# Performance work log

Measured on AMD Instinct MI355X. Metric: run time of the kernel, lower is better.

The kernel has to match this reference:

```python
import jax, jax.numpy as jnp
import numpy as np

PD_THR = 1e-6  # positive-definiteness floor for the diagonal covariance

N_IN, DIM, BATCH = 8192, 128, 4096


def setup_inputs() -> dict:
    key = jax.random.key(0)
    kx, km = jax.random.split(key)
    x = jax.random.normal(kx, (BATCH, DIM), dtype=jnp.float32)
    mean = jax.random.normal(km, (N_IN, DIM), dtype=jnp.float32)
    diag = jnp.ones((N_IN, DIM), dtype=jnp.float32)
    return {"x": x, "mean": mean, "diag": diag}


def reference(x, mean, diag):
    """Energies[b, i] = KL( N(x_b, I) || N(mean_i, diag(diag_i)) ).

    Diagonal-Gaussian KL:
      0.5 * sum_d [ log(diag_id) + (1 + (x_bd - mu_id)^2) / diag_id - 1 ]

    The pairwise quadratic term is expanded into GEMMs to avoid the
    (batch, n_in, dim) broadcast intermediate:
      sum_d (x-mu)^2/diag = x^2 @ inv.T - 2 x @ (mu*inv).T + sum(mu^2*inv)
    Returns (batch, n_in), i.e. the original's energies.T.
    """
    d = jnp.clip(diag, PD_THR, None)              # (n_in, dim)
    inv = 1.0 / d                                 # (n_in, dim)
    # pairwise Mahalanobis quadratic, shape (batch, n_in)
    quad = (
        (x * x) @ inv.T
        - 2.0 * (x @ (mean * inv).T)
        + jnp.sum(mean * mean * inv, axis=-1)     # (n_in,) broadcast
    )
    # per-codebook constants: logdet + trace(inv) - dim
    const = jnp.sum(jnp.log(d), axis=-1) + jnp.sum(inv, axis=-1) - x.shape[-1]
    return 0.5 * (quad + const)                   # (batch, n_in)
```

## Files before the change

kernel.cpp:

```cpp
#include <hip/hip_runtime.h>
#include <hip/hip_bf16.h>


#define BATCH 4096
#define N_IN  8192
#define DIM   128
#define KP    768
#define PD_THR 1e-6f

#define BM 256
#define BN 256
#define BK 64
#define NT (KP / BK)

typedef __attribute__((ext_vector_type(4))) float f32x4;
typedef __attribute__((ext_vector_type(8))) short bf16x8;

static __device__ __forceinline__ unsigned short f2bf(float v) {
    union { __hip_bfloat16 h; unsigned short u; } cv;
    cv.h = __float2bfloat16(v);
    return cv.u;
}
static __device__ __forceinline__ float bf2f(unsigned short u) {
    union { unsigned short u; __hip_bfloat16 h; } cv;
    cv.u = u;
    return __bfloat162float(cv.h);
}

__global__ void prep_a_kernel(const float* __restrict__ x,
                              unsigned short* __restrict__ Ap) {
    int t = blockIdx.x * 256 + threadIdx.x;
    int row = t >> 7;
    int d   = t & 127;
    float v  = x[t];
    float x2 = v * v;
    unsigned short x2h = f2bf(x2);
    unsigned short x2l = f2bf(x2 - bf2f(x2h));
    unsigned short xh  = f2bf(v);
    unsigned short xl  = f2bf(v - bf2f(xh));
    unsigned short* a = Ap + (size_t)row * KP;
    a[d]       = x2h;  a[128 + d] = xh;
    a[256 + d] = x2h;  a[384 + d] = xh;
    a[512 + d] = x2l;  a[640 + d] = xl;
}

__global__ void prep_b_kernel(const float* __restrict__ mean,
                              const float* __restrict__ diag,
                              unsigned short* __restrict__ Bp,
                              float* __restrict__ cvec) {
    int wave = threadIdx.x >> 6, lane = threadIdx.x & 63;
    int row = blockIdx.x * 4 + wave;
    const float* mrow = mean + (size_t)row * DIM;
    const float* drow = diag + (size_t)row * DIM;
    unsigned short* b = Bp + (size_t)row * KP;
    float csum = 0.0f;
#pragma unroll
    for (int j = 0; j < 2; ++j) {
        int d = lane + 64 * j;
        float m   = mrow[d];
        float dd  = fmaxf(drow[d], PD_THR);
        float inv = 1.0f / dd;
        float fm  = -2.0f * m * inv;
        csum += m * m * inv + logf(dd) + inv;
        unsigned short ih = f2bf(inv);
        unsigned short il = f2bf(inv - bf2f(ih));
        unsigned short fh = f2bf(fm);
        unsigned short fl = f2bf(fm - bf2f(fh));
        b[d]       = ih;  b[128 + d] = fh;
        b[256 + d] = il;  b[384 + d] = fl;
        b[512 + d] = ih;  b[640 + d] = fh;
    }
#pragma unroll
    for (int off = 32; off > 0; off >>= 1) csum += __shfl_down(csum, off);
    if (lane == 0) cvec[row] = csum - (float)DIM;
}

__global__ void __launch_bounds__(512, 2)
kl_gemm(const unsigned short* __restrict__ Ap,
        const unsigned short* __restrict__ Bp,
        const float* __restrict__ cvec,
        float* __restrict__ out) {
    __shared__ __align__(16) unsigned short lds[2][2 * BM * BK];

    int bid0 = blockIdx.x;
    int bid  = (bid0 & 7) * 64 + (bid0 >> 3);
    int bx = bid & 15;
    int by = bid >> 4;
    int m0 = bx * BM, n0 = by * BN;

    int tid  = threadIdx.x;
    int wave = tid >> 6, lane = tid & 63;
    int wr = wave >> 2, wc = wave & 3;

    const int lrow  = lane >> 3;
    const int lslot = (lane & 7) ^ lrow;

    const unsigned short* gA = Ap + (size_t)(m0 + wave * 8 + lrow) * KP + lslot * 8;
    const unsigned short* gB = Bp + (size_t)(n0 + wave * 8 + lrow) * KP + lslot * 8;

    f32x4 acc[8][4];
#pragma unroll
    for (int m = 0; m < 8; ++m)
#pragma unroll
        for (int n = 0; n < 4; ++n) acc[m][n] = (f32x4){0.f, 0.f, 0.f, 0.f};

    auto STAGE = [&](int b, int t) {
        int k0 = t * BK;
#pragma unroll
        for (int j = 0; j < 4; ++j)
            __builtin_amdgcn_global_load_lds(
                (const __attribute__((address_space(1))) void*)(gA + (size_t)j * 64 * KP + k0),
                (__attribute__((address_space(3))) void*)&lds[b][(wave * 8 + j * 64) * 64],
                16, 0, 0);
#pragma unroll
        for (int j = 0; j < 4; ++j)
            __builtin_amdgcn_global_load_lds(
                (const __attribute__((address_space(1))) void*)(gB + (size_t)j * 64 * KP + k0),
                (__attribute__((address_space(3))) void*)&lds[b][16384 + (wave * 8 + j * 64) * 64],
                16, 0, 0);
    };

    auto COMPUTE = [&](int b) {
        const unsigned short* La = &lds[b][0];
        const unsigned short* Lb = &lds[b][16384];
#pragma unroll
        for (int kk = 0; kk < BK; kk += 32) {
            const int phys = (((kk >> 3) + (lane >> 4)) ^ (lane & 7)) * 8;
            bf16x8 af[8], bf[4];
#pragma unroll
            for (int m = 0; m < 8; ++m)
                af[m] = *(const bf16x8*)&La[(wr * 128 + m * 16 + (lane & 15)) * 64 + phys];
#pragma unroll
            for (int n = 0; n < 4; ++n)
                bf[n] = *(const bf16x8*)&Lb[(wc * 64 + n * 16 + (lane & 15)) * 64 + phys];
            __builtin_amdgcn_s_setprio(1);
#pragma unroll
            for (int m = 0; m < 8; ++m)
#pragma unroll
                for (int n = 0; n < 4; ++n)
                    acc[m][n] = __builtin_amdgcn_mfma_f32_16x16x32_bf16(
                        af[m], bf[n], acc[m][n], 0, 0, 0);
            __builtin_amdgcn_s_setprio(0);
        }
    };

    STAGE(0, 0);
    STAGE(1, 1);
#pragma unroll 1
    for (int t = 0; t < NT - 1; ++t) {
        asm volatile("s_waitcnt vmcnt(8)" ::: "memory");
        __builtin_amdgcn_s_barrier();
        __builtin_amdgcn_sched_barrier(0);
        COMPUTE(t & 1);
        __builtin_amdgcn_s_barrier();
        __builtin_amdgcn_sched_barrier(0);
        if (t + 2 < NT) STAGE(t & 1, t + 2);
    }
    asm volatile("s_waitcnt vmcnt(0)" ::: "memory");
    __builtin_amdgcn_s_barrier();
    __builtin_amdgcn_sched_barrier(0);
    COMPUTE((NT - 1) & 1);
    __builtin_amdgcn_s_barrier();
    __builtin_amdgcn_sched_barrier(0);

    float* lbw = (float*)&lds[0][0] + wave * 1024;
    const int crow0 = m0 + wr * 128;
    const int ccol0 = n0 + wc * 64;
    const int lr = (lane >> 4) << 2;
    const int lc = lane & 15;
#pragma unroll
    for (int m = 0; m < 8; ++m) {
#pragma unroll
        for (int n = 0; n < 4; ++n)
#pragma unroll
            for (int r = 0; r < 4; ++r)
                lbw[(lr + r) * 64 + n * 16 + lc] = acc[m][n][r];
#pragma unroll
        for (int q = 0; q < 4; ++q) {
            int flat = q * 256 + lane * 4;
            int row  = flat >> 6;
            int col  = flat & 63;
            f32x4 v  = *(const f32x4*)&lbw[flat];
            f32x4 c4 = *(const f32x4*)&cvec[ccol0 + col];
            f32x4 o  = (v + c4) * 0.5f;
            __builtin_nontemporal_store(
                o, (f32x4*)&out[(size_t)(crow0 + m * 16 + row) * N_IN + ccol0 + col]);
        }
    }
}

extern "C" void kernel_launch(void* const* d_in, const int* in_sizes, int n_in_args,
                              void* d_out, int out_size, void* d_ws, size_t ws_size,
                              hipStream_t stream) {
    (void)in_sizes; (void)n_in_args; (void)out_size; (void)ws_size;
    const float* x    = (const float*)d_in[0];
    const float* mean = (const float*)d_in[1];
    const float* diag = (const float*)d_in[2];
    float* out = (float*)d_out;

    char* ws = (char*)d_ws;
    unsigned short* Bp = (unsigned short*)ws;
    unsigned short* Ap = (unsigned short*)(ws + (size_t)N_IN * KP * 2);
    float* cvec = (float*)(ws + (size_t)N_IN * KP * 2 + (size_t)BATCH * KP * 2);

    prep_a_kernel<<<BATCH * DIM / 256, 256, 0, stream>>>(x, Ap);
    prep_b_kernel<<<N_IN / 4, 256, 0, stream>>>(mean, diag, Bp, cvec);
    kl_gemm<<<(BATCH / BM) * (N_IN / BN), 512, 0, stream>>>(Ap, Bp, cvec, out);
}
```

Measured before the change: 209.5 us.

## Drop B low-part split terms and shrink K from 768 to 512 with B reuse

Switches from a 3-term bf16 split (hi*hi + hi*lo + lo*hi) to a 2-term split in which only A carries a low part. B is stored once at K=256 and reloaded by wrapping its K offset, so A is 512 wide. This removes a third of the MFMA work and shrinks B traffic and workspace, at the cost of accuracy because inv and -2*mean*inv are now rounded to bf16 with no correction. The block-to-tile mapping is also changed so that each XCD covers a compact 8x8 group of tiles, which should improve L2 reuse.

```diff
diff --git a/kernel.cpp b/kernel.cpp
--- a/kernel.cpp
+++ b/kernel.cpp
@@ -5,13 +5,14 @@
 #define BATCH 4096
 #define N_IN  8192
 #define DIM   128
-#define KP    768
+#define KPA   512
+#define KPB   256
 #define PD_THR 1e-6f
 
 #define BM 256
 #define BN 256
 #define BK 64
-#define NT (KP / BK)
+#define NT (KPA / BK)
 
 typedef __attribute__((ext_vector_type(4))) float f32x4;
 typedef __attribute__((ext_vector_type(8))) short bf16x8;
@@ -38,10 +39,9 @@
     unsigned short x2l = f2bf(x2 - bf2f(x2h));
     unsigned short xh  = f2bf(v);
     unsigned short xl  = f2bf(v - bf2f(xh));
-    unsigned short* a = Ap + (size_t)row * KP;
+    unsigned short* a = Ap + (size_t)row * KPA;
     a[d]       = x2h;  a[128 + d] = xh;
-    a[256 + d] = x2h;  a[384 + d] = xh;
-    a[512 + d] = x2l;  a[640 + d] = xl;
+    a[256 + d] = x2l;  a[384 + d] = xl;
 }
 
 __global__ void prep_b_kernel(const float* __restrict__ mean,
@@ -52,7 +52,7 @@
     int row = blockIdx.x * 4 + wave;
     const float* mrow = mean + (size_t)row * DIM;
     const float* drow = diag + (size_t)row * DIM;
-    unsigned short* b = Bp + (size_t)row * KP;
+    unsigned short* b = Bp + (size_t)row * KPB;
     float csum = 0.0f;
 #pragma unroll
     for (int j = 0; j < 2; ++j) {
@@ -62,13 +62,8 @@
         float inv = 1.0f / dd;
         float fm  = -2.0f * m * inv;
         csum += m * m * inv + logf(dd) + inv;
-        unsigned short ih = f2bf(inv);
-        unsigned short il = f2bf(inv - bf2f(ih));
-        unsigned short fh = f2bf(fm);
-        unsigned short fl = f2bf(fm - bf2f(fh));
-        b[d]       = ih;  b[128 + d] = fh;
-        b[256 + d] = il;  b[384 + d] = fl;
-        b[512 + d] = ih;  b[640 + d] = fh;
+        b[d]       = f2bf(inv);
+        b[128 + d] = f2bf(fm);
     }
 #pragma unroll
     for (int off = 32; off > 0; off >>= 1) csum += __shfl_down(csum, off);
@@ -83,9 +78,9 @@
     __shared__ __align__(16) unsigned short lds[2][2 * BM * BK];
 
     int bid0 = blockIdx.x;
-    int bid  = (bid0 & 7) * 64 + (bid0 >> 3);
-    int bx = bid & 15;
-    int by = bid >> 4;
+    int xcd = bid0 & 7, g = bid0 >> 3;
+    int bx = (xcd & 1) * 8 + (g & 7);
+    int by = (xcd >> 1) * 8 + (g >> 3);
     int m0 = bx * BM, n0 = by * BN;
 
     int tid  = threadIdx.x;
@@ -95,8 +90,8 @@
     const int lrow  = lane >> 3;
     const int lslot = (lane & 7) ^ lrow;
 
-    const unsigned short* gA = Ap + (size_t)(m0 + wave * 8 + lrow) * KP + lslot * 8;
-    const unsigned short* gB = Bp + (size_t)(n0 + wave * 8 + lrow) * KP + lslot * 8;
+    const unsigned short* gA = Ap + (size_t)(m0 + wave * 8 + lrow) * KPA + lslot * 8;
+    const unsigned short* gB = Bp + (size_t)(n0 + wave * 8 + lrow) * KPB + lslot * 8;
 
     f32x4 acc[8][4];
 #pragma unroll
@@ -105,17 +100,18 @@
         for (int n = 0; n < 4; ++n) acc[m][n] = (f32x4){0.f, 0.f, 0.f, 0.f};
 
     auto STAGE = [&](int b, int t) {
-        int k0 = t * BK;
+        int k0a = t * BK;
+        int k0b = (t & 3) * BK;
 #pragma unroll
         for (int j = 0; j < 4; ++j)
             __builtin_amdgcn_global_load_lds(
-                (const __attribute__((address_space(1))) void*)(gA + (size_t)j * 64 * KP + k0),
+                (const __attribute__((address_space(1))) void*)(gA + (size_t)j * 64 * KPA + k0a),
                 (__attribute__((address_space(3))) void*)&lds[b][(wave * 8 + j * 64) * 64],
                 16, 0, 0);
 #pragma unroll
         for (int j = 0; j < 4; ++j)
             __builtin_amdgcn_global_load_lds(
-                (const __attribute__((address_space(1))) void*)(gB + (size_t)j * 64 * KP + k0),
+                (const __attribute__((address_space(1))) void*)(gB + (size_t)j * 64 * KPB + k0b),
                 (__attribute__((address_space(3))) void*)&lds[b][16384 + (wave * 8 + j * 64) * 64],
                 16, 0, 0);
     };
@@ -125,7 +121,7 @@
         const unsigned short* Lb = &lds[b][16384];
 #pragma unroll
         for (int kk = 0; kk < BK; kk += 32) {
-            const int phys = (((kk >> 3) + (lane >> 4)) ^ (lane & 7)) * 8;
+            const int phys = ((((kk >> 3) + (lane >> 4))) ^ (lane & 7)) * 8;
             bf16x8 af[8], bf[4];
 #pragma unroll
             for (int m = 0; m < 8; ++m)
@@ -200,8 +196,8 @@
 
     char* ws = (char*)d_ws;
     unsigned short* Bp = (unsigned short*)ws;
-    unsigned short* Ap = (unsigned short*)(ws + (size_t)N_IN * KP * 2);
-    float* cvec = (float*)(ws + (size_t)N_IN * KP * 2 + (size_t)BATCH * KP * 2);
+    unsigned short* Ap = (unsigned short*)(ws + (size_t)N_IN * KPB * 2);
+    float* cvec = (float*)(ws + (size_t)N_IN * KPB * 2 + (size_t)BATCH * KPA * 2);
 
     prep_a_kernel<<<BATCH * DIM / 256, 256, 0, stream>>>(x, Ap);
     prep_b_kernel<<<N_IN / 4, 256, 0, stream>>>(mean, diag, Bp, cvec);
```

New measurement: 188.9 us. 1.11x faster.
